# Kernel tuning notes

Measured on AMD Instinct MI355X. Metric: run time of the kernel, lower is better.

The kernel has to match this reference:

```python
import jax, jax.numpy as jnp
import numpy as np

H = 64  # hidden size


def _gru_cell(x, h, Wih, Whh, bih, bhh):
    """PyTorch-convention GRU cell. x:[B,in], h:[B,H]. Gate order: r, z, n."""
    gi = x @ Wih.T + bih              # [B, 3H]
    gh = h @ Whh.T + bhh              # [B, 3H]
    ir, iz, in_ = jnp.split(gi, 3, axis=-1)
    hr, hz, hn = jnp.split(gh, 3, axis=-1)
    r = jax.nn.sigmoid(ir + hr)
    z = jax.nn.sigmoid(iz + hz)
    n = jnp.tanh(in_ + r * hn)
    return (1.0 - z) * n + z * h


def setup_inputs() -> dict:
    key = jax.random.key(0)
    B, T, NIN = 4096, 256, 6
    ks = jax.random.split(key, 24)

    def w(k, shape, fan):
        return (jax.random.normal(k, shape, jnp.float32) / np.sqrt(fan).astype(np.float32))

    inp = {"x": jax.random.normal(ks[0], (B, T, NIN), jnp.float32)}
    # encoder layer 0 (input 6) and layer 1 (input 64)
    inp["enc_Wih0"] = w(ks[1], (3 * H, NIN), H)
    inp["enc_Whh0"] = w(ks[2], (3 * H, H), H)
    inp["enc_bih0"] = w(ks[3], (3 * H,), H)
    inp["enc_bhh0"] = w(ks[4], (3 * H,), H)
    inp["enc_Wih1"] = w(ks[5], (3 * H, H), H)
    inp["enc_Whh1"] = w(ks[6], (3 * H, H), H)
    inp["enc_bih1"] = w(ks[7], (3 * H,), H)
    inp["enc_bhh1"] = w(ks[8], (3 * H,), H)
    # decoder layer 0 (input 1) and layer 1 (input 64)
    inp["dec_Wih0"] = w(ks[9], (3 * H, 1), H)
    inp["dec_Whh0"] = w(ks[10], (3 * H, H), H)
    inp["dec_bih0"] = w(ks[11], (3 * H,), H)
    inp["dec_bhh0"] = w(ks[12], (3 * H,), H)
    inp["dec_Wih1"] = w(ks[13], (3 * H, H), H)
    inp["dec_Whh1"] = w(ks[14], (3 * H, H), H)
    inp["dec_bih1"] = w(ks[15], (3 * H,), H)
    inp["dec_bhh1"] = w(ks[16], (3 * H,), H)
    # output head
    inp["out_W"] = w(ks[17], (1, H), H)
    inp["out_b"] = w(ks[18], (1,), H)
    inp["target_len"] = 180
    return inp


def reference(x, enc_Wih0, enc_Whh0, enc_bih0, enc_bhh0,
              enc_Wih1, enc_Whh1, enc_bih1, enc_bhh1,
              dec_Wih0, dec_Whh0, dec_bih0, dec_bhh0,
              dec_Wih1, dec_Whh1, dec_bih1, dec_bhh1,
              out_W, out_b, target_len):
    B = x.shape[0]
    dtype = x.dtype

    # ---- encoder: 2-layer GRU over x, return final hidden per layer ----
    seq = jnp.swapaxes(x, 0, 1)  # [T, B, 6] time-major
    enc_layers = [(enc_Wih0, enc_Whh0, enc_bih0, enc_bhh0),
                  (enc_Wih1, enc_Whh1, enc_bih1, enc_bhh1)]
    h_finals = []
    for (Wih, Whh, bih, bhh) in enc_layers:
        def step(h, xt, Wih=Wih, Whh=Whh, bih=bih, bhh=bhh):
            hn = _gru_cell(xt, h, Wih, Whh, bih, bhh)
            return hn, hn
        h_last, seq = jax.lax.scan(step, jnp.zeros((B, H), dtype), seq)
        h_finals.append(h_last)

    def dec_step(carry, _):
        h0, h1, prev = carry
        h0 = _gru_cell(prev, h0, dec_Wih0, dec_Whh0, dec_bih0, dec_bhh0)
        h1 = _gru_cell(h0, h1, dec_Wih1, dec_Whh1, dec_bih1, dec_bhh1)
        cv = h1 @ out_W.T + out_b  # [B, 1]
        return (h0, h1, cv), cv

    prev0 = jnp.zeros((B, 1), dtype)
    _, outs = jax.lax.scan(dec_step, (h_finals[0], h_finals[1], prev0),
                           None, length=target_len)
    return jnp.swapaxes(outs, 0, 1)  # [B, target_len, 1]
```

## Files before the change

### kernel.cpp

```cpp
#include <hip/hip_runtime.h>
#include <cstdint>

typedef _Float16 half8 __attribute__((ext_vector_type(8)));
typedef __attribute__((ext_vector_type(4))) float floatx4;
typedef unsigned int uint;

#define TSEQ 256
#define TDEC 180
#define NIN  6
#define GROWS 16
#define NBLK (4096 / GROWS)
#define RS0 104
#define RS1 72
#define L2E 1.4426950408889634f

__device__ __forceinline__ floatx4 mfma16(half8 a, half8 b, floatx4 c) {
  return __builtin_amdgcn_mfma_f32_16x16x32_f16(a, b, c, 0, 0, 0);
}

__device__ __forceinline__ float sigm2(float v) {
  return __builtin_amdgcn_rcpf(1.0f + __builtin_amdgcn_exp2f(-v));
}
__device__ __forceinline__ float tanh2(float v) {
  return fmaf(2.0f, __builtin_amdgcn_rcpf(1.0f + __builtin_amdgcn_exp2f(-v)), -1.0f);
}

__device__ __forceinline__ half8 ldh8(const _Float16* p) { return *(const half8*)p; }

#define PASS2_I3(F0, F1, r, z, g, W, QR, QZ, QG) do {                   \
  r = mfma16(F0, W[0][0], QR); z = mfma16(F0, W[1][0], QZ); g = mfma16(F0, W[2][0], QG); \
  r = mfma16(F1, W[0][1], r);  z = mfma16(F1, W[1][1], z);  g = mfma16(F1, W[2][1], g);  \
} while (0)

#define PASS2_A2I1(F0, F1, r, z, g, W, QG) do {                         \
  r = mfma16(F0, W[0][0], r); z = mfma16(F0, W[1][0], z); g = mfma16(F0, W[2][0], QG); \
  r = mfma16(F1, W[0][1], r); z = mfma16(F1, W[1][1], z); g = mfma16(F1, W[2][1], g);  \
} while (0)

#define PASS1_A2I1(F0, r, z, g, W, QG) do {                             \
  r = mfma16(F0, W[0][0], r); z = mfma16(F0, W[1][0], z); g = mfma16(F0, W[2][0], QG); \
} while (0)

__device__ __forceinline__ void pollge1(const volatile uint* p, uint need4) {
  for (;;) {
    if (*p >= need4) break;
    __builtin_amdgcn_s_sleep(1);
  }
  asm volatile("" ::: "memory");
}

#define PUBLISH() do { asm volatile("" ::: "memory"); if (lane == 0) atomicAdd(mysum, 1u); } while (0)

__global__ void __launch_bounds__(512, 2)
gru_persist(const float* __restrict__ x,
            const float* __restrict__ eWih0, const float* __restrict__ eWhh0,
            const float* __restrict__ ebih0, const float* __restrict__ ebhh0,
            const float* __restrict__ eWih1, const float* __restrict__ eWhh1,
            const float* __restrict__ ebih1, const float* __restrict__ ebhh1,
            const float* __restrict__ dWih0, const float* __restrict__ dWhh0,
            const float* __restrict__ dbih0, const float* __restrict__ dbhh0,
            const float* __restrict__ dWih1, const float* __restrict__ dWhh1,
            const float* __restrict__ dbih1, const float* __restrict__ dbhh1,
            const float* __restrict__ outW, const float* __restrict__ outB,
            float* __restrict__ out)
{
  __shared__ __align__(16) _Float16 s0[2][16][RS0];
  __shared__ __align__(16) _Float16 s1[2][16][RS1];
  __shared__ __align__(16) uint prog[16];

  const int tid  = threadIdx.x;
  const bool isA = tid < 256;
  const int wvL  = (tid >> 6) & 3;
  const int lane = tid & 63;
  const int c    = lane & 15;
  const int q    = lane >> 4;
  const int u    = wvL * 16 + c;
  const long base = (long)blockIdx.x * GROWS;

  const volatile uint* asum = (const volatile uint*)&prog[0];
  const volatile uint* bsum = (const volatile uint*)&prog[8];
  uint* mysum = (uint*)&prog[isA ? 0 : 8];

  for (int i = tid; i < 2 * 16 * RS0; i += 512) ((uint16_t*)s0)[i] = 0;
  for (int i = tid; i < 2 * 16 * RS1; i += 512) ((uint16_t*)s1)[i] = 0;
  if (tid < 16) prog[tid] = 0;
  if (tid < GROWS * NIN) {
    int m = tid / 6, i2 = tid - m * 6;
    s0[0][m][64 + i2] = (_Float16)x[(base + m) * (TSEQ * NIN) + i2];
  }

  half8 W1[3][2];
  half8 W2[3][2];
  float hr[4] = {0, 0, 0, 0};
  const float SC[3] = {L2E, L2E, 2.0f * L2E};

  auto loadW64 = [&](const float* W, half8 (&D)[3][2]) {
    #pragma unroll
    for (int s = 0; s < 3; s++) {
      const int n = (s * 4 + wvL) * 16 + c;
      #pragma unroll
      for (int kt = 0; kt < 2; kt++) {
        const int k0 = kt * 32 + q * 8;
        #pragma unroll
        for (int j = 0; j < 8; j++) D[s][kt][j] = (_Float16)(SC[s] * W[n * 64 + k0 + j]);
      }
    }
  };

  float cR, cZ, c3, c4;
  if (isA) {
    loadW64(eWhh0, W1);
    #pragma unroll
    for (int s = 0; s < 3; s++) {
      const int n = (s * 4 + wvL) * 16 + c;
      #pragma unroll
      for (int kt = 0; kt < 2; kt++)
        #pragma unroll
        for (int j = 0; j < 8; j++) {
          float v = (kt == 0 && q == 0 && j < NIN) ? SC[s] * eWih0[n * NIN + j] : 0.0f;
          W2[s][kt][j] = (_Float16)v;
        }
    }
    cR = L2E * (ebih0[u] + ebhh0[u]);
    cZ = L2E * (ebih0[64 + u] + ebhh0[64 + u]);
    c3 = 2.0f * L2E * ebhh0[128 + u];
    c4 = 2.0f * L2E * ebih0[128 + u];
  } else {
    loadW64(eWih1, W1); loadW64(eWhh1, W2);
    cR = L2E * (ebih1[u] + ebhh1[u]);
    cZ = L2E * (ebih1[64 + u] + ebhh1[64 + u]);
    c3 = 2.0f * L2E * ebih1[128 + u];
    c4 = 2.0f * L2E * ebhh1[128 + u];
  }
  __syncthreads();

  if (isA) {
    floatx4 QR = {cR, cR, cR, cR}, QZ = {cZ, cZ, cZ, cZ};
    floatx4 Q3 = {c3, c3, c3, c3}, Q4 = {c4, c4, c4, c4};
    const bool doX = (wvL == 0) && (lane < 48);
    const float *px0 = nullptr, *px1 = nullptr;
    int xo0 = 0, xo1 = 0; float xn0 = 0.f, xn1 = 0.f;
    if (doX) {
      int s0_ = lane, s1_ = lane + 48;
      int m0 = s0_ / 6, i0 = s0_ - m0 * 6, m1 = s1_ / 6, i1 = s1_ - m1 * 6;
      px0 = x + (base + m0) * (TSEQ * NIN) + i0;
      px1 = x + (base + m1) * (TSEQ * NIN) + i1;
      xo0 = m0 * RS0 + 64 + i0; xo1 = m1 * RS0 + 64 + i1;
      xn0 = px0[NIN]; xn1 = px1[NIN];
    }
    for (int i = 0; i < TSEQ; i += 2) {
      #pragma unroll
      for (int h2 = 0; h2 < 2; h2++) {
        const int i_ = i + h2, p = h2, pn = h2 ^ 1;
        pollge1(asum, 4u * (uint)i_);
        const half8 a0 = ldh8(&s0[p][c][q * 8]);
        const half8 a1 = ldh8(&s0[p][c][32 + q * 8]);
        const half8 xf = ldh8(&s0[p][c][64 + q * 8]);
        floatx4 aR, aZ, a3, a4;
        PASS2_I3(a0, a1, aR, aZ, a3, W1, QR, QZ, Q3);
        PASS1_A2I1(xf, aR, aZ, a4, W2, Q4);
        pollge1(bsum, 4u * (uint)(i_ > 0 ? i_ - 1 : 0));
        if (doX && i_ + 1 < TSEQ) {
          ((_Float16*)s0[pn])[xo0] = (_Float16)xn0;
          ((_Float16*)s0[pn])[xo1] = (_Float16)xn1;
          if (i_ + 2 < TSEQ) { xn0 = px0[(i_ + 2) * NIN]; xn1 = px1[(i_ + 2) * NIN]; }
        }
        #pragma unroll
        for (int r4 = 0; r4 < 4; r4++) {
          const float gr = sigm2(aR[r4]);
          const float gz = sigm2(aZ[r4]);
          const float nn = tanh2(a4[r4] + gr * a3[r4]);
          const float hn = nn + gz * (hr[r4] - nn);
          hr[r4] = hn;
          s0[pn][q * 4 + r4][u] = (_Float16)hn;
        }
        PUBLISH();
      }
    }
    loadW64(dWhh0, W1);
    const float ob = outB[0];
    #pragma unroll
    for (int s = 0; s < 3; s++) {
      const int n = (s * 4 + wvL) * 16 + c;
      const float wd = SC[s] * dWih0[n];
      #pragma unroll
      for (int kt = 0; kt < 2; kt++) {
        const int k0 = kt * 32 + q * 8;
        #pragma unroll
        for (int j = 0; j < 8; j++) W2[s][kt][j] = (_Float16)(wd * outW[k0 + j]);
      }
    }
    const float bR0 = L2E * (dbih0[u] + dbhh0[u]);
    const float bZ0 = L2E * (dbih0[64 + u] + dbhh0[64 + u]);
    const float b30 = 2.0f * L2E * dbhh0[128 + u];
    const float b40 = 2.0f * L2E * dbih0[128 + u];
    cR = bR0 + L2E * (dWih0[u] * ob);
    cZ = bZ0 + L2E * (dWih0[64 + u] * ob);
    c3 = b30;
    c4 = b40 + 2.0f * L2E * (dWih0[128 + u] * ob);
    QR = (floatx4){cR, cR, cR, cR}; QZ = (floatx4){cZ, cZ, cZ, cZ};
    Q3 = (floatx4){c3, c3, c3, c3}; Q4 = (floatx4){c4, c4, c4, c4};
    {
      pollge1(asum, 4u * (uint)TSEQ);
      const half8 a0 = ldh8(&s0[0][c][q * 8]);
      const half8 a1 = ldh8(&s0[0][c][32 + q * 8]);
      const floatx4 TR = {bR0, bR0, bR0, bR0}, TZ = {bZ0, bZ0, bZ0, bZ0};
      const floatx4 T3 = {b30, b30, b30, b30};
      floatx4 aR, aZ, a3;
      floatx4 a4 = {b40, b40, b40, b40};
      PASS2_I3(a0, a1, aR, aZ, a3, W1, TR, TZ, T3);
      pollge1(bsum, 4u * (uint)(TSEQ - 1));
      #pragma unroll
      for (int r4 = 0; r4 < 4; r4++) {
        const float gr = sigm2(aR[r4]);
        const float gz = sigm2(aZ[r4]);
        const float nn = tanh2(a4[r4] + gr * a3[r4]);
        const float hn = nn + gz * (hr[r4] - nn);
        hr[r4] = hn;
        s0[1][q * 4 + r4][u] = (_Float16)hn;
      }
      PUBLISH();
    }
    {
      pollge1(asum, 4u * (uint)(TSEQ + 1));
      const half8 a0 = ldh8(&s0[1][c][q * 8]);
      const half8 a1 = ldh8(&s0[1][c][32 + q * 8]);
      floatx4 aR, aZ, a3, a4;
      PASS2_I3(a0, a1, aR, aZ, a3, W1, QR, QZ, Q3);
      pollge1(bsum, 4u * (uint)(TSEQ + 1));
      const half8 b0 = ldh8(&s1[1][c][q * 8]);
      const half8 b1 = ldh8(&s1[1][c][32 + q * 8]);
      PASS2_A2I1(b0, b1, aR, aZ, a4, W2, Q4);
      #pragma unroll
      for (int r4 = 0; r4 < 4; r4++) {
        const float gr = sigm2(aR[r4]);
        const float gz = sigm2(aZ[r4]);
        const float nn = tanh2(a4[r4] + gr * a3[r4]);
        const float hn = nn + gz * (hr[r4] - nn);
        hr[r4] = hn;
        s0[0][q * 4 + r4][u] = (_Float16)hn;
      }
      PUBLISH();
    }
    for (int i = TSEQ + 2; i < TSEQ + TDEC; i += 2) {
      #pragma unroll
      for (int h2 = 0; h2 < 2; h2++) {
        const int i_ = i + h2, p = h2, pn = h2 ^ 1;
        pollge1(asum, 4u * (uint)i_);
        const half8 a0 = ldh8(&s0[p][c][q * 8]);
        const half8 a1 = ldh8(&s0[p][c][32 + q * 8]);
        floatx4 aR, aZ, a3, a4;
        PASS2_I3(a0, a1, aR, aZ, a3, W1, QR, QZ, Q3);
        pollge1(bsum, 4u * (uint)i_);
        const half8 b0 = ldh8(&s1[p][c][q * 8]);
        const half8 b1 = ldh8(&s1[p][c][32 + q * 8]);
        PASS2_A2I1(b0, b1, aR, aZ, a4, W2, Q4);
        #pragma unroll
        for (int r4 = 0; r4 < 4; r4++) {
          const float gr = sigm2(aR[r4]);
          const float gz = sigm2(aZ[r4]);
          const float nn = tanh2(a4[r4] + gr * a3[r4]);
          const float hn = nn + gz * (hr[r4] - nn);
          hr[r4] = hn;
          s0[pn][q * 4 + r4][u] = (_Float16)hn;
        }
        PUBLISH();
      }
    }
  } else {
    floatx4 QR = {cR, cR, cR, cR}, QZ = {cZ, cZ, cZ, cZ};
    floatx4 Q3 = {c3, c3, c3, c3}, Q4 = {c4, c4, c4, c4};
    const float ob = outB[0];
    float wk[2][8];
    #pragma unroll
    for (int kt = 0; kt < 2; kt++)
      #pragma unroll
      for (int j = 0; j < 8; j++) wk[kt][j] = outW[kt * 32 + q * 8 + j];

    for (int i = 0; i < TSEQ; i += 2) {
      #pragma unroll
      for (int h2 = 0; h2 < 2; h2++) {
        const int i_ = i + h2, p = h2, pn = h2 ^ 1;
        pollge1(bsum, 4u * (uint)i_);
        const half8 f0 = ldh8(&s1[p][c][q * 8]);
        const half8 f1 = ldh8(&s1[p][c][32 + q * 8]);
        floatx4 aR, aZ, a3, a4;
        PASS2_I3(f0, f1, aR, aZ, a4, W2, QR, QZ, Q4);
        pollge1(asum, 4u * (uint)(i_ + 1));
        const half8 g0 = ldh8(&s0[pn][c][q * 8]);
        const half8 g1 = ldh8(&s0[pn][c][32 + q * 8]);
        PASS2_A2I1(g0, g1, aR, aZ, a3, W1, Q3);
        #pragma unroll
        for (int r4 = 0; r4 < 4; r4++) {
          const float gr = sigm2(aR[r4]);
          const float gz = sigm2(aZ[r4]);
          const float nn = tanh2(a3[r4] + gr * a4[r4]);
          const float hn = nn + gz * (hr[r4] - nn);
          hr[r4] = hn;
          s1[pn][q * 4 + r4][u] = (_Float16)hn;
        }
        PUBLISH();
      }
    }
    loadW64(dWih1, W1); loadW64(dWhh1, W2);
    cR = L2E * (dbih1[u] + dbhh1[u]);
    cZ = L2E * (dbih1[64 + u] + dbhh1[64 + u]);
    c3 = 2.0f * L2E * dbih1[128 + u];
    c4 = 2.0f * L2E * dbhh1[128 + u];
    QR = (floatx4){cR, cR, cR, cR}; QZ = (floatx4){cZ, cZ, cZ, cZ};
    Q3 = (floatx4){c3, c3, c3, c3}; Q4 = (floatx4){c4, c4, c4, c4};
    for (int i = TSEQ; i < TSEQ + TDEC; i += 2) {
      #pragma unroll
      for (int h2 = 0; h2 < 2; h2++) {
        const int i_ = i + h2, p = h2, pn = h2 ^ 1;
        pollge1(bsum, 4u * (uint)i_);
        const half8 f0 = ldh8(&s1[p][c][q * 8]);
        const half8 f1 = ldh8(&s1[p][c][32 + q * 8]);
        floatx4 aR, aZ, a3, a4;
        PASS2_I3(f0, f1, aR, aZ, a4, W2, QR, QZ, Q4);
        if (wvL == 0 && i_ > TSEQ) {
          float cv = 0.0f;
          #pragma unroll
          for (int j = 0; j < 8; j++) {
            cv = fmaf((float)f0[j], wk[0][j], cv);
            cv = fmaf((float)f1[j], wk[1][j], cv);
          }
          cv += __shfl_xor(cv, 16);
          cv += __shfl_xor(cv, 32);
          if (lane < 16) out[(base + lane) * TDEC + (i_ - TSEQ - 1)] = cv + ob;
        }
        pollge1(asum, 4u * (uint)(i_ + 1));
        const half8 g0 = ldh8(&s0[pn][c][q * 8]);
        const half8 g1 = ldh8(&s0[pn][c][32 + q * 8]);
        PASS2_A2I1(g0, g1, aR, aZ, a3, W1, Q3);
        #pragma unroll
        for (int r4 = 0; r4 < 4; r4++) {
          const float gr = sigm2(aR[r4]);
          const float gz = sigm2(aZ[r4]);
          const float nn = tanh2(a3[r4] + gr * a4[r4]);
          const float hn = nn + gz * (hr[r4] - nn);
          hr[r4] = hn;
          s1[pn][q * 4 + r4][u] = (_Float16)hn;
        }
        PUBLISH();
      }
    }
    if (wvL == 0) {
      pollge1(bsum, 4u * (uint)(TSEQ + TDEC));
      const half8 f0 = ldh8(&s1[0][c][q * 8]);
      const half8 f1 = ldh8(&s1[0][c][32 + q * 8]);
      float cv = 0.0f;
      #pragma unroll
      for (int j = 0; j < 8; j++) {
        cv = fmaf((float)f0[j], wk[0][j], cv);
        cv = fmaf((float)f1[j], wk[1][j], cv);
      }
      cv += __shfl_xor(cv, 16);
      cv += __shfl_xor(cv, 32);
      if (lane < 16) out[(base + lane) * TDEC + (TDEC - 1)] = cv + ob;
    }
  }
}

extern "C" void kernel_launch(void* const* d_in, const int* in_sizes, int n_in,
                              void* d_out, int out_size, void* d_ws, size_t ws_size,
                              hipStream_t stream) {
  (void)in_sizes; (void)n_in; (void)d_ws; (void)ws_size; (void)out_size;
  const float* x     = (const float*)d_in[0];
  const float* eWih0 = (const float*)d_in[1];
  const float* eWhh0 = (const float*)d_in[2];
  const float* ebih0 = (const float*)d_in[3];
  const float* ebhh0 = (const float*)d_in[4];
  const float* eWih1 = (const float*)d_in[5];
  const float* eWhh1 = (const float*)d_in[6];
  const float* ebih1 = (const float*)d_in[7];
  const float* ebhh1 = (const float*)d_in[8];
  const float* dWih0 = (const float*)d_in[9];
  const float* dWhh0 = (const float*)d_in[10];
  const float* dbih0 = (const float*)d_in[11];
  const float* dbhh0 = (const float*)d_in[12];
  const float* dWih1 = (const float*)d_in[13];
  const float* dWhh1 = (const float*)d_in[14];
  const float* dbih1 = (const float*)d_in[15];
  const float* dbhh1 = (const float*)d_in[16];
  const float* outW  = (const float*)d_in[17];
  const float* outB  = (const float*)d_in[18];
  hipLaunchKernelGGL(gru_persist, dim3(NBLK), dim3(512), 0, stream,
                     x, eWih0, eWhh0, ebih0, ebhh0, eWih1, eWhh1, ebih1, ebhh1,
                     dWih0, dWhh0, dbih0, dbhh0, dWih1, dWhh1, dbih1, dbhh1,
                     outW, outB, (float*)d_out);
}
```

Baseline: 392.7 us.

## Quadruple-buffer hidden state to loosen encoder layer coupling and preload decoder weights

Hidden-state buffers in LDS grow from 2 to 4 slots. During the encoder, layer 0 now waits only until layer 1 is three steps behind rather than one, so the two wave groups can drift further apart. The x prefetch is deepened to two steps ahead. Decoder weights and biases are now loaded into separate registers up front, which removes the mid-kernel reload between phases but doubles weight register use and may lower occupancy or cause spills at 512 threads with 2 blocks per CU. The decoder loops become un-unrolled single-step loops with modulo-4 slot indexing.

Measured after the change: 387.1 us. Within noise of the previous version (-1.4%).

```diff
diff --git a/kernel.cpp b/kernel.cpp
--- a/kernel.cpp
+++ b/kernel.cpp
@@ -10,6 +10,7 @@
 #define NIN  6
 #define GROWS 16
 #define NBLK (4096 / GROWS)
+#define NSL 4
 #define RS0 104
 #define RS1 72
 #define L2E 1.4426950408889634f
@@ -64,8 +65,8 @@
             const float* __restrict__ outW, const float* __restrict__ outB,
             float* __restrict__ out)
 {
-  __shared__ __align__(16) _Float16 s0[2][16][RS0];
-  __shared__ __align__(16) _Float16 s1[2][16][RS1];
+  __shared__ __align__(16) _Float16 s0[NSL][16][RS0];
+  __shared__ __align__(16) _Float16 s1[NSL][16][RS1];
   __shared__ __align__(16) uint prog[16];
 
   const int tid  = threadIdx.x;
@@ -81,16 +82,16 @@
   const volatile uint* bsum = (const volatile uint*)&prog[8];
   uint* mysum = (uint*)&prog[isA ? 0 : 8];
 
-  for (int i = tid; i < 2 * 16 * RS0; i += 512) ((uint16_t*)s0)[i] = 0;
-  for (int i = tid; i < 2 * 16 * RS1; i += 512) ((uint16_t*)s1)[i] = 0;
+  for (int i = tid; i < NSL * 16 * RS0; i += 512) ((uint16_t*)s0)[i] = 0;
+  for (int i = tid; i < NSL * 16 * RS1; i += 512) ((uint16_t*)s1)[i] = 0;
   if (tid < 16) prog[tid] = 0;
   if (tid < GROWS * NIN) {
     int m = tid / 6, i2 = tid - m * 6;
     s0[0][m][64 + i2] = (_Float16)x[(base + m) * (TSEQ * NIN) + i2];
   }
 
-  half8 W1[3][2];
-  half8 W2[3][2];
+  half8 W1[3][2], W2[3][2];
+  half8 W1d[3][2], W2d[3][2];
   float hr[4] = {0, 0, 0, 0};
   const float SC[3] = {L2E, L2E, 2.0f * L2E};
 
@@ -107,7 +108,11 @@
     }
   };
 
+  const float ob = outB[0];
   float cR, cZ, c3, c4;
+  float dR, dZ, d3, d4;
+  float bR0 = 0, bZ0 = 0, b30 = 0, b40 = 0;
+  float wk[2][8];
   if (isA) {
     loadW64(eWhh0, W1);
     #pragma unroll
@@ -121,16 +126,45 @@
           W2[s][kt][j] = (_Float16)v;
         }
     }
+    loadW64(dWhh0, W1d);
+    #pragma unroll
+    for (int s = 0; s < 3; s++) {
+      const int n = (s * 4 + wvL) * 16 + c;
+      const float wd = SC[s] * dWih0[n];
+      #pragma unroll
+      for (int kt = 0; kt < 2; kt++) {
+        const int k0 = kt * 32 + q * 8;
+        #pragma unroll
+        for (int j = 0; j < 8; j++) W2d[s][kt][j] = (_Float16)(wd * outW[k0 + j]);
+      }
+    }
     cR = L2E * (ebih0[u] + ebhh0[u]);
     cZ = L2E * (ebih0[64 + u] + ebhh0[64 + u]);
     c3 = 2.0f * L2E * ebhh0[128 + u];
     c4 = 2.0f * L2E * ebih0[128 + u];
+    bR0 = L2E * (dbih0[u] + dbhh0[u]);
+    bZ0 = L2E * (dbih0[64 + u] + dbhh0[64 + u]);
+    b30 = 2.0f * L2E * dbhh0[128 + u];
+    b40 = 2.0f * L2E * dbih0[128 + u];
+    dR = bR0 + L2E * (dWih0[u] * ob);
+    dZ = bZ0 + L2E * (dWih0[64 + u] * ob);
+    d3 = b30;
+    d4 = b40 + 2.0f * L2E * (dWih0[128 + u] * ob);
   } else {
     loadW64(eWih1, W1); loadW64(eWhh1, W2);
+    loadW64(dWih1, W1d); loadW64(dWhh1, W2d);
     cR = L2E * (ebih1[u] + ebhh1[u]);
     cZ = L2E * (ebih1[64 + u] + ebhh1[64 + u]);
     c3 = 2.0f * L2E * ebih1[128 + u];
     c4 = 2.0f * L2E * ebhh1[128 + u];
+    dR = L2E * (dbih1[u] + dbhh1[u]);
+    dZ = L2E * (dbih1[64 + u] + dbhh1[64 + u]);
+    d3 = 2.0f * L2E * dbih1[128 + u];
+    d4 = 2.0f * L2E * dbhh1[128 + u];
+    #pragma unroll
+    for (int kt = 0; kt < 2; kt++)
+      #pragma unroll
+      for (int j = 0; j < 8; j++) wk[kt][j] = outW[kt * 32 + q * 8 + j];
   }
   __syncthreads();
 
@@ -139,19 +173,21 @@
     floatx4 Q3 = {c3, c3, c3, c3}, Q4 = {c4, c4, c4, c4};
     const bool doX = (wvL == 0) && (lane < 48);
     const float *px0 = nullptr, *px1 = nullptr;
-    int xo0 = 0, xo1 = 0; float xn0 = 0.f, xn1 = 0.f;
+    int xo0 = 0, xo1 = 0;
+    float xa0 = 0.f, xa1 = 0.f, xb0 = 0.f, xb1 = 0.f;
     if (doX) {
       int s0_ = lane, s1_ = lane + 48;
       int m0 = s0_ / 6, i0 = s0_ - m0 * 6, m1 = s1_ / 6, i1 = s1_ - m1 * 6;
       px0 = x + (base + m0) * (TSEQ * NIN) + i0;
       px1 = x + (base + m1) * (TSEQ * NIN) + i1;
       xo0 = m0 * RS0 + 64 + i0; xo1 = m1 * RS0 + 64 + i1;
-      xn0 = px0[NIN]; xn1 = px1[NIN];
-    }
-    for (int i = 0; i < TSEQ; i += 2) {
-      #pragma unroll
-      for (int h2 = 0; h2 < 2; h2++) {
-        const int i_ = i + h2, p = h2, pn = h2 ^ 1;
+      xa0 = px0[NIN];     xa1 = px1[NIN];
+      xb0 = px0[2 * NIN]; xb1 = px1[2 * NIN];
+    }
+    for (int i = 0; i < TSEQ; i += 4) {
+      #pragma unroll
+      for (int h4 = 0; h4 < 4; h4++) {
+        const int i_ = i + h4, p = h4, pn = (h4 + 1) & 3;
         pollge1(asum, 4u * (uint)i_);
         const half8 a0 = ldh8(&s0[p][c][q * 8]);
         const half8 a1 = ldh8(&s0[p][c][32 + q * 8]);
@@ -159,11 +195,12 @@
         floatx4 aR, aZ, a3, a4;
         PASS2_I3(a0, a1, aR, aZ, a3, W1, QR, QZ, Q3);
         PASS1_A2I1(xf, aR, aZ, a4, W2, Q4);
-        pollge1(bsum, 4u * (uint)(i_ > 0 ? i_ - 1 : 0));
+        pollge1(bsum, 4u * (uint)(i_ > 3 ? i_ - 3 : 0));
         if (doX && i_ + 1 < TSEQ) {
-          ((_Float16*)s0[pn])[xo0] = (_Float16)xn0;
-          ((_Float16*)s0[pn])[xo1] = (_Float16)xn1;
-          if (i_ + 2 < TSEQ) { xn0 = px0[(i_ + 2) * NIN]; xn1 = px1[(i_ + 2) * NIN]; }
+          ((_Float16*)s0[pn])[xo0] = (_Float16)xa0;
+          ((_Float16*)s0[pn])[xo1] = (_Float16)xa1;
+          xa0 = xb0; xa1 = xb1;
+          if (i_ + 3 < TSEQ) { xb0 = px0[(i_ + 3) * NIN]; xb1 = px1[(i_ + 3) * NIN]; }
         }
         #pragma unroll
         for (int r4 = 0; r4 < 4; r4++) {
@@ -177,29 +214,8 @@
         PUBLISH();
       }
     }
-    loadW64(dWhh0, W1);
-    const float ob = outB[0];
-    #pragma unroll
-    for (int s = 0; s < 3; s++) {
-      const int n = (s * 4 + wvL) * 16 + c;
-      const float wd = SC[s] * dWih0[n];
-      #pragma unroll
-      for (int kt = 0; kt < 2; kt++) {
-        const int k0 = kt * 32 + q * 8;
-        #pragma unroll
-        for (int j = 0; j < 8; j++) W2[s][kt][j] = (_Float16)(wd * outW[k0 + j]);
-      }
-    }
-    const float bR0 = L2E * (dbih0[u] + dbhh0[u]);
-    const float bZ0 = L2E * (dbih0[64 + u] + dbhh0[64 + u]);
-    const float b30 = 2.0f * L2E * dbhh0[128 + u];
-    const float b40 = 2.0f * L2E * dbih0[128 + u];
-    cR = bR0 + L2E * (dWih0[u] * ob);
-    cZ = bZ0 + L2E * (dWih0[64 + u] * ob);
-    c3 = b30;
-    c4 = b40 + 2.0f * L2E * (dWih0[128 + u] * ob);
-    QR = (floatx4){cR, cR, cR, cR}; QZ = (floatx4){cZ, cZ, cZ, cZ};
-    Q3 = (floatx4){c3, c3, c3, c3}; Q4 = (floatx4){c4, c4, c4, c4};
+    QR = (floatx4){dR, dR, dR, dR}; QZ = (floatx4){dZ, dZ, dZ, dZ};
+    Q3 = (floatx4){d3, d3, d3, d3}; Q4 = (floatx4){d4, d4, d4, d4};
     {
       pollge1(asum, 4u * (uint)TSEQ);
       const half8 a0 = ldh8(&s0[0][c][q * 8]);
@@ -208,7 +224,7 @@
       const floatx4 T3 = {b30, b30, b30, b30};
       floatx4 aR, aZ, a3;
       floatx4 a4 = {b40, b40, b40, b40};
-      PASS2_I3(a0, a1, aR, aZ, a3, W1, TR, TZ, T3);
+      PASS2_I3(a0, a1, aR, aZ, a3, W1d, TR, TZ, T3);
       pollge1(bsum, 4u * (uint)(TSEQ - 1));
       #pragma unroll
       for (int r4 = 0; r4 < 4; r4++) {
@@ -221,16 +237,17 @@
       }
       PUBLISH();
     }
-    {
-      pollge1(asum, 4u * (uint)(TSEQ + 1));
-      const half8 a0 = ldh8(&s0[1][c][q * 8]);
-      const half8 a1 = ldh8(&s0[1][c][32 + q * 8]);
+    for (int i_ = TSEQ + 1; i_ < TSEQ + TDEC; i_++) {
+      const int p = i_ & 3, pn = (i_ + 1) & 3;
+      pollge1(asum, 4u * (uint)i_);
+      const half8 a0 = ldh8(&s0[p][c][q * 8]);
+      const half8 a1 = ldh8(&s0[p][c][32 + q * 8]);
       floatx4 aR, aZ, a3, a4;
-      PASS2_I3(a0, a1, aR, aZ, a3, W1, QR, QZ, Q3);
-      pollge1(bsum, 4u * (uint)(TSEQ + 1));
-      const half8 b0 = ldh8(&s1[1][c][q * 8]);
-      const half8 b1 = ldh8(&s1[1][c][32 + q * 8]);
-      PASS2_A2I1(b0, b1, aR, aZ, a4, W2, Q4);
+      PASS2_I3(a0, a1, aR, aZ, a3, W1d, QR, QZ, Q3);
+      pollge1(bsum, 4u * (uint)i_);
+      const half8 b0 = ldh8(&s1[p][c][q * 8]);
+      const half8 b1 = ldh8(&s1[p][c][32 + q * 8]);
+      PASS2_A2I1(b0, b1, aR, aZ, a4, W2d, Q4);
       #pragma unroll
       for (int r4 = 0; r4 < 4; r4++) {
         const float gr = sigm2(aR[r4]);
@@ -238,49 +255,17 @@
         const float nn = tanh2(a4[r4] + gr * a3[r4]);
         const float hn = nn + gz * (hr[r4] - nn);
         hr[r4] = hn;
-        s0[0][q * 4 + r4][u] = (_Float16)hn;
+        s0[pn][q * 4 + r4][u] = (_Float16)hn;
       }
       PUBLISH();
-    }
-    for (int i = TSEQ + 2; i < TSEQ + TDEC; i += 2) {
-      #pragma unroll
-      for (int h2 = 0; h2 < 2; h2++) {
-        const int i_ = i + h2, p = h2, pn = h2 ^ 1;
-        pollge1(asum, 4u * (uint)i_);
-        const half8 a0 = ldh8(&s0[p][c][q * 8]);
-        const half8 a1 = ldh8(&s0[p][c][32 + q * 8]);
-        floatx4 aR, aZ, a3, a4;
-        PASS2_I3(a0, a1, aR, aZ, a3, W1, QR, QZ, Q3);
-        pollge1(bsum, 4u * (uint)i_);
-        const half8 b0 = ldh8(&s1[p][c][q * 8]);
-        const half8 b1 = ldh8(&s1[p][c][32 + q * 8]);
-        PASS2_A2I1(b0, b1, aR, aZ, a4, W2, Q4);
-        #pragma unroll
-        for (int r4 = 0; r4 < 4; r4++) {
-          const float gr = sigm2(aR[r4]);
-          const float gz = sigm2(aZ[r4]);
-          const float nn = tanh2(a4[r4] + gr * a3[r4]);
-          const float hn = nn + gz * (hr[r4] - nn);
-          hr[r4] = hn;
-          s0[pn][q * 4 + r4][u] = (_Float16)hn;
-        }
-        PUBLISH();
-      }
     }
   } else {
     floatx4 QR = {cR, cR, cR, cR}, QZ = {cZ, cZ, cZ, cZ};
     floatx4 Q3 = {c3, c3, c3, c3}, Q4 = {c4, c4, c4, c4};
-    const float ob = outB[0];
-    float wk[2][8];
-    #pragma unroll
-    for (int kt = 0; kt < 2; kt++)
-      #pragma unroll
-      for (int j = 0; j < 8; j++) wk[kt][j] = outW[kt * 32 + q * 8 + j];
-
-    for (int i = 0; i < TSEQ; i += 2) {
-      #pragma unroll
-      for (int h2 = 0; h2 < 2; h2++) {
-        const int i_ = i + h2, p = h2, pn = h2 ^ 1;
+    for (int i = 0; i < TSEQ; i += 4) {
+      #pragma unroll
+      for (int h4 = 0; h4 < 4; h4++) {
+        const int i_ = i + h4, p = h4, pn = (h4 + 1) & 3;
         pollge1(bsum, 4u * (uint)i_);
         const half8 f0 = ldh8(&s1[p][c][q * 8]);
         const half8 f1 = ldh8(&s1[p][c][32 + q * 8]);
@@ -302,48 +287,40 @@
         PUBLISH();
       }
     }
-    loadW64(dWih1, W1); loadW64(dWhh1, W2);
-    cR = L2E * (dbih1[u] + dbhh1[u]);
-    cZ = L2E * (dbih1[64 + u] + dbhh1[64 + u]);
-    c3 = 2.0f * L2E * dbih1[128 + u];
-    c4 = 2.0f * L2E * dbhh1[128 + u];
-    QR = (floatx4){cR, cR, cR, cR}; QZ = (floatx4){cZ, cZ, cZ, cZ};
-    Q3 = (floatx4){c3, c3, c3, c3}; Q4 = (floatx4){c4, c4, c4, c4};
-    for (int i = TSEQ; i < TSEQ + TDEC; i += 2) {
-      #pragma unroll
-      for (int h2 = 0; h2 < 2; h2++) {
-        const int i_ = i + h2, p = h2, pn = h2 ^ 1;
-        pollge1(bsum, 4u * (uint)i_);
-        const half8 f0 = ldh8(&s1[p][c][q * 8]);
-        const half8 f1 = ldh8(&s1[p][c][32 + q * 8]);
-        floatx4 aR, aZ, a3, a4;
-        PASS2_I3(f0, f1, aR, aZ, a4, W2, QR, QZ, Q4);
-        if (wvL == 0 && i_ > TSEQ) {
-          float cv = 0.0f;
-          #pragma unroll
-          for (int j = 0; j < 8; j++) {
-            cv = fmaf((float)f0[j], wk[0][j], cv);
-            cv = fmaf((float)f1[j], wk[1][j], cv);
-          }
-          cv += __shfl_xor(cv, 16);
-          cv += __shfl_xor(cv, 32);
-          if (lane < 16) out[(base + lane) * TDEC + (i_ - TSEQ - 1)] = cv + ob;
-        }
-        pollge1(asum, 4u * (uint)(i_ + 1));
-        const half8 g0 = ldh8(&s0[pn][c][q * 8]);
-        const half8 g1 = ldh8(&s0[pn][c][32 + q * 8]);
-        PASS2_A2I1(g0, g1, aR, aZ, a3, W1, Q3);
-        #pragma unroll
-        for (int r4 = 0; r4 < 4; r4++) {
-          const float gr = sigm2(aR[r4]);
-          const float gz = sigm2(aZ[r4]);
-          const float nn = tanh2(a3[r4] + gr * a4[r4]);
-          const float hn = nn + gz * (hr[r4] - nn);
-          hr[r4] = hn;
-          s1[pn][q * 4 + r4][u] = (_Float16)hn;
-        }
-        PUBLISH();
-      }
+    QR = (floatx4){dR, dR, dR, dR}; QZ = (floatx4){dZ, dZ, dZ, dZ};
+    Q3 = (floatx4){d3, d3, d3, d3}; Q4 = (floatx4){d4, d4, d4, d4};
+    for (int i_ = TSEQ; i_ < TSEQ + TDEC; i_++) {
+      const int p = i_ & 3, pn = (i_ + 1) & 3;
+      pollge1(bsum, 4u * (uint)i_);
+      const half8 f0 = ldh8(&s1[p][c][q * 8]);
+      const half8 f1 = ldh8(&s1[p][c][32 + q * 8]);
+      floatx4 aR, aZ, a3, a4;
+      PASS2_I3(f0, f1, aR, aZ, a4, W2d, QR, QZ, Q4);
+      if (wvL == 0 && i_ > TSEQ) {
+        float cv = 0.0f;
+        #pragma unroll
+        for (int j = 0; j < 8; j++) {
+          cv = fmaf((float)f0[j], wk[0][j], cv);
+          cv = fmaf((float)f1[j], wk[1][j], cv);
+        }
+        cv += __shfl_xor(cv, 16);
+        cv += __shfl_xor(cv, 32);
+        if (lane < 16) out[(base + lane) * TDEC + (i_ - TSEQ - 1)] = cv + ob;
+      }
+      pollge1(asum, 4u * (uint)(i_ + 1));
+      const half8 g0 = ldh8(&s0[pn][c][q * 8]);
+      const half8 g1 = ldh8(&s0[pn][c][32 + q * 8]);
+      PASS2_A2I1(g0, g1, aR, aZ, a3, W1d, Q3);
+      #pragma unroll
+      for (int r4 = 0; r4 < 4; r4++) {
+        const float gr = sigm2(aR[r4]);
+        const float gz = sigm2(aZ[r4]);
+        const float nn = tanh2(a3[r4] + gr * a4[r4]);
+        const float hn = nn + gz * (hr[r4] - nn);
+        hr[r4] = hn;
+        s1[pn][q * 4 + r4][u] = (_Float16)hn;
+      }
+      PUBLISH();
     }
     if (wvL == 0) {
       pollge1(bsum, 4u * (uint)(TSEQ + TDEC));
```
